# Performance work log

Hardware: AMD Instinct MI355X
Metric: run time of the kernel (lower is better)

Reference implementation:

```python
import jax, jax.numpy as jnp
import numpy as np

N = 50000
E = 800000
F_IN = 1433
H = 256
C = 7


def setup_inputs() -> dict:
    key = jax.random.key(0)
    ks = jax.random.split(key, 8)
    x = jax.random.normal(ks[0], (N, F_IN), dtype=jnp.float32)
    edge_index = jax.random.randint(ks[1], (2, E), 0, N, dtype=jnp.int32)
    # glorot init for linear weights
    def glorot(k, fan_in, fan_out):
        s = jnp.sqrt(6.0 / (fan_in + fan_out)).astype(jnp.float32)
        return jax.random.uniform(k, (fan_in, fan_out), jnp.float32, -s, s)
    W1 = glorot(ks[2], F_IN, H)
    W2 = glorot(ks[3], H, H)
    W3 = glorot(ks[4], H, C)
    b1 = jnp.zeros((H,), jnp.float32)
    b2 = jnp.zeros((H,), jnp.float32)
    b3 = jnp.zeros((C,), jnp.float32)
    return {"x": x, "edge_index": edge_index, "W1": W1, "b1": b1,
            "W2": W2, "b2": b2, "W3": W3, "b3": b3}


def _gcn_norm(edge_index, num_nodes):
    # add self-loops, edge_weight = 1, symmetric normalization
    row = jnp.concatenate([edge_index[0], jnp.arange(num_nodes, dtype=edge_index.dtype)])
    col = jnp.concatenate([edge_index[1], jnp.arange(num_nodes, dtype=edge_index.dtype)])
    w = jnp.ones(row.shape[0], dtype=jnp.float32)
    deg = jax.ops.segment_sum(w, col, num_segments=num_nodes)  # degree on target (col)
    dinv = jnp.where(deg > 0, jax.lax.rsqrt(deg), 0.0)
    norm = dinv[row] * dinv[col]  # [E+N]
    return row, col, norm


def _gcn_layer(x, W, b, row, col, norm, num_nodes):
    h = x @ W                                   # [N, F_out]
    msg = h[row] * norm[:, None]                # gather + scale, [E+N, F_out]
    out = jax.ops.segment_sum(msg, col, num_segments=num_nodes)  # scatter-add
    return out + b


def reference(x, edge_index, W1, b1, W2, b2, W3, b3):
    row, col, norm = _gcn_norm(edge_index, N)
    h = jax.nn.relu(_gcn_layer(x, W1, b1, row, col, norm, N))
    h = jax.nn.relu(_gcn_layer(h, W2, b2, row, col, norm, N))
    h = _gcn_layer(h, W3, b3, row, col, norm, N)
    return jax.nn.log_softmax(h, axis=1)
```

## Files before the change

kernel.cpp:

```cpp
#include <hip/hip_runtime.h>
#include <math.h>

#define NNODES 50000
#define NEDGES 800000
#define FIN    1433
#define KP1    1472
#define HDIM   256
#define NCLS   7
#define MPAD   50048

typedef __attribute__((ext_vector_type(8))) short short8;
typedef __attribute__((ext_vector_type(4))) float f32x4;

__device__ __forceinline__ unsigned short f2bf(float f) {
    unsigned u = __builtin_bit_cast(unsigned, f);
    u += 0x7fffu + ((u >> 16) & 1u);
    return (unsigned short)(u >> 16);
}

__device__ __forceinline__ float bf2f(unsigned short u) {
    unsigned v = ((unsigned)u) << 16;
    return __builtin_bit_cast(float, v);
}

__device__ __forceinline__ void gl2lds16(const void* g, void* l) {
    __builtin_amdgcn_global_load_lds(
        (const __attribute__((address_space(1))) unsigned int*)g,
        (__attribute__((address_space(3))) unsigned int*)l, 16, 0, 0);
}

__device__ __forceinline__ f32x4 ld4u(const float* p) {
    f32x4 v; __builtin_memcpy(&v, p, 16); return v;
}


__global__ void count_kernel(const int* __restrict__ col, int* __restrict__ cnt, int E) {
    int e = blockIdx.x * blockDim.x + threadIdx.x;
    if (e < E) atomicAdd(&cnt[col[e]], 1);
}

#define SCAN_BS 512

__global__ __launch_bounds__(SCAN_BS) void scan_part(const int* __restrict__ cnt,
                                                     int* __restrict__ bsum, int n) {
    __shared__ int red[SCAN_BS];
    int t = threadIdx.x;
    int i = blockIdx.x * SCAN_BS + t;
    red[t] = (i < n) ? cnt[i] : 0;
    __syncthreads();
    for (int off = SCAN_BS / 2; off > 0; off >>= 1) {
        if (t < off) red[t] += red[t + off];
        __syncthreads();
    }
    if (t == 0) bsum[blockIdx.x] = red[0];
}

__global__ __launch_bounds__(128) void scan_top(int* __restrict__ bsum, int nb) {
    __shared__ int s[128];
    int t = threadIdx.x;
    int v = (t < nb) ? bsum[t] : 0;
    s[t] = v;
    __syncthreads();
    for (int off = 1; off < 128; off <<= 1) {
        int u = (t >= off) ? s[t - off] : 0;
        __syncthreads();
        s[t] += u;
        __syncthreads();
    }
    if (t < nb) bsum[t] = s[t] - v;
}

__global__ __launch_bounds__(SCAN_BS) void scan_apply(const int* __restrict__ cnt,
                                                      const int* __restrict__ bsum,
                                                      int* __restrict__ rp,
                                                      float* __restrict__ dinv,
                                                      int n, int total) {
    __shared__ int s[SCAN_BS];
    int t = threadIdx.x;
    int i = blockIdx.x * SCAN_BS + t;
    int v = (i < n) ? cnt[i] : 0;
    s[t] = v;
    __syncthreads();
    for (int off = 1; off < SCAN_BS; off <<= 1) {
        int u = (t >= off) ? s[t - off] : 0;
        __syncthreads();
        s[t] += u;
        __syncthreads();
    }
    if (i < n) {
        rp[i] = bsum[blockIdx.x] + s[t] - v;
        dinv[i] = rsqrtf((float)(v + 1));
    }
    if (i == n) rp[n] = total;
}

__global__ void fill_kernel(const int* __restrict__ row, const int* __restrict__ col,
                            const int* __restrict__ rp, int* __restrict__ cur,
                            int2* __restrict__ csrw,
                            const float* __restrict__ dinv, int E) {
    int e = blockIdx.x * blockDim.x + threadIdx.x;
    if (e < E) {
        int c = col[e], r = row[e];
        int pos = rp[c] + atomicAdd(&cur[c], 1);
        csrw[pos] = make_int2(r, __float_as_int(dinv[r] * dinv[c]));
    }
}


__global__ void cast_wt2(const float* __restrict__ W1, const float* __restrict__ W2,
                         unsigned short* __restrict__ w1t, unsigned short* __restrict__ w2t) {
    int idx = blockIdx.x * blockDim.x + threadIdx.x;
    if (idx < HDIM * KP1) {
        int n = idx / KP1, k = idx % KP1;
        w1t[idx] = f2bf((k < FIN) ? W1[(size_t)k * HDIM + n] : 0.f);
    } else {
        int j = idx - HDIM * KP1;
        if (j < HDIM * HDIM) {
            int n = j / HDIM, k = j % HDIM;
            w2t[j] = f2bf(W2[(size_t)k * HDIM + n]);
        }
    }
}


__global__ __launch_bounds__(256) void gemm1_fused(const float* __restrict__ X,
                                                   const unsigned short* __restrict__ Bt,
                                                   unsigned short* __restrict__ C) {
    __shared__ __align__(16) unsigned short As[64 * 64];
    __shared__ __align__(16) unsigned short Bs[256 * 64];
    const int tid = threadIdx.x;
    const int wave = tid >> 6, lane = tid & 63;
    const int m0 = blockIdx.x * 64;
    const int wn = wave * 64;
    const int kq = lane >> 4, l16 = lane & 15;
    const int lq = lane >> 4;
    const int h  = lane & 15;

    int rowbase[4];
    #pragma unroll
    for (int i = 0; i < 4; ++i) {
        int r = m0 + wave * 16 + i * 4 + lq;
        if (r >= NNODES) r = NNODES - 1;
        rowbase[i] = r * FIN;
    }
    int aw[4];
    #pragma unroll
    for (int i = 0; i < 4; ++i) {
        int r7 = lq + 4 * (i & 1);
        aw[i] = (wave * 16 + i * 4 + lq) * 64 + (((h >> 1) ^ r7) * 8) + (h & 1) * 4;
    }

    int bo[8];
    #pragma unroll
    for (int i = 0; i < 8; ++i) {
        int c = i * 256 + tid;
        int n = c >> 3, ccg = (c & 7) ^ (n & 7);
        bo[i] = n * KP1 + ccg * 8;
    }

    int aoffb[2], boffb[2];
    #pragma unroll
    for (int ks = 0; ks < 2; ++ks) {
        int swz = ((ks * 4 + kq) ^ (l16 & 7)) * 8;
        aoffb[ks] = l16 * 64 + swz;
        boffb[ks] = (wn + l16) * 64 + swz;
    }

    f32x4 acc[4][4] = {};
    constexpr int NT = KP1 / 64;

    f32x4 fv[4];
    #pragma unroll
    for (int i = 0; i < 4; ++i) fv[i] = ld4u(&X[rowbase[i] + h * 4]);

    for (int t = 0; t < NT; ++t) {
        const int k0 = t * 64;
        #pragma unroll
        for (int i = 0; i < 8; ++i)
            gl2lds16(Bt + bo[i] + k0, &Bs[(i * 256 + tid) * 8]);
        #pragma unroll
        for (int i = 0; i < 4; ++i) {
            ushort4 pk = make_ushort4(f2bf(fv[i].x), f2bf(fv[i].y),
                                      f2bf(fv[i].z), f2bf(fv[i].w));
            *(ushort4*)&As[aw[i]] = pk;
        }
        __syncthreads();

        f32x4 nv[4];
        const bool more = (t + 1 < NT);
        if (more) {
            const int kb = k0 + 64 + h * 4;
            if (t + 2 == NT) {
                #pragma unroll
                for (int i = 0; i < 4; ++i) {
                    float a = (kb + 0 < FIN) ? X[rowbase[i] + kb + 0] : 0.f;
                    float b = (kb + 1 < FIN) ? X[rowbase[i] + kb + 1] : 0.f;
                    float c = (kb + 2 < FIN) ? X[rowbase[i] + kb + 2] : 0.f;
                    float d = (kb + 3 < FIN) ? X[rowbase[i] + kb + 3] : 0.f;
                    nv[i] = (f32x4){a, b, c, d};
                }
            } else {
                #pragma unroll
                for (int i = 0; i < 4; ++i) nv[i] = ld4u(&X[rowbase[i] + kb]);
            }
        }

        #pragma unroll
        for (int ks = 0; ks < 2; ++ks) {
            short8 af[4], bg[4];
            #pragma unroll
            for (int i = 0; i < 4; ++i) af[i] = *(const short8*)&As[i * 1024 + aoffb[ks]];
            #pragma unroll
            for (int j = 0; j < 4; ++j) bg[j] = *(const short8*)&Bs[j * 1024 + boffb[ks]];
            #pragma unroll
            for (int i = 0; i < 4; ++i)
                #pragma unroll
                for (int j = 0; j < 4; ++j)
                    acc[i][j] = __builtin_amdgcn_mfma_f32_16x16x32_bf16(af[i], bg[j], acc[i][j], 0, 0, 0);
        }
        __syncthreads();
        if (more) {
            #pragma unroll
            for (int i = 0; i < 4; ++i) fv[i] = nv[i];
        }
    }

    #pragma unroll
    for (int i = 0; i < 4; ++i) {
        int gm_base = m0 + i * 16 + (lane >> 4) * 4;
        #pragma unroll
        for (int r = 0; r < 4; ++r) {
            int gm = gm_base + r;
            if (gm < NNODES) {
                #pragma unroll
                for (int j = 0; j < 4; ++j) {
                    int gn = wn + j * 16 + l16;
                    C[(size_t)gm * HDIM + gn] = f2bf(acc[i][j][r]);
                }
            }
        }
    }
}


__global__ __launch_bounds__(256) void gemm2_lds(const unsigned short* __restrict__ A,
                                                 const unsigned short* __restrict__ Bt,
                                                 unsigned short* __restrict__ C) {
    __shared__ __align__(16) unsigned short As[64 * 64];
    __shared__ __align__(16) unsigned short Bs[256 * 64];
    const int tid = threadIdx.x;
    const int wave = tid >> 6, lane = tid & 63;
    const int m0 = blockIdx.x * 64;
    const int wn = wave * 64;
    const int kq = lane >> 4, l16 = lane & 15;

    int ao[2];
    #pragma unroll
    for (int i = 0; i < 2; ++i) {
        int c = i * 256 + tid;
        int m = c >> 3, ccg = (c & 7) ^ (m & 7);
        ao[i] = (m0 + m) * HDIM + ccg * 8;
    }
    int bo[8];
    #pragma unroll
    for (int i = 0; i < 8; ++i) {
        int c = i * 256 + tid;
        int n = c >> 3, ccg = (c & 7) ^ (n & 7);
        bo[i] = n * HDIM + ccg * 8;
    }
    int aoffb[2], boffb[2];
    #pragma unroll
    for (int ks = 0; ks < 2; ++ks) {
        int swz = ((ks * 4 + kq) ^ (l16 & 7)) * 8;
        aoffb[ks] = l16 * 64 + swz;
        boffb[ks] = (wn + l16) * 64 + swz;
    }

    f32x4 acc[4][4] = {};
    #pragma unroll
    for (int k0 = 0; k0 < HDIM; k0 += 64) {
        #pragma unroll
        for (int i = 0; i < 2; ++i) gl2lds16(A + ao[i] + k0, &As[(i * 256 + tid) * 8]);
        #pragma unroll
        for (int i = 0; i < 8; ++i) gl2lds16(Bt + bo[i] + k0, &Bs[(i * 256 + tid) * 8]);
        __syncthreads();
        #pragma unroll
        for (int ks = 0; ks < 2; ++ks) {
            short8 af[4], bg[4];
            #pragma unroll
            for (int i = 0; i < 4; ++i) af[i] = *(const short8*)&As[i * 1024 + aoffb[ks]];
            #pragma unroll
            for (int j = 0; j < 4; ++j) bg[j] = *(const short8*)&Bs[j * 1024 + boffb[ks]];
            #pragma unroll
            for (int i = 0; i < 4; ++i)
                #pragma unroll
                for (int j = 0; j < 4; ++j)
                    acc[i][j] = __builtin_amdgcn_mfma_f32_16x16x32_bf16(af[i], bg[j], acc[i][j], 0, 0, 0);
        }
        __syncthreads();
    }

    #pragma unroll
    for (int i = 0; i < 4; ++i) {
        int gm_base = m0 + i * 16 + (lane >> 4) * 4;
        #pragma unroll
        for (int r = 0; r < 4; ++r) {
            int gm = gm_base + r;
            if (gm < NNODES) {
                #pragma unroll
                for (int j = 0; j < 4; ++j) {
                    int gn = wn + j * 16 + l16;
                    C[(size_t)gm * HDIM + gn] = f2bf(acc[i][j][r]);
                }
            }
        }
    }
}


__device__ __forceinline__ void aggregate_row(const ushort4* __restrict__ h, int lane,
                                              int p, int p1,
                                              const int2* __restrict__ csrw,
                                              float& ax, float& ay, float& az, float& aw) {
    for (; p + 8 <= p1; p += 8) {
        int2 e[8];
        #pragma unroll
        for (int j = 0; j < 8; ++j) e[j] = csrw[p + j];
        ushort4 t[8];
        #pragma unroll
        for (int j = 0; j < 8; ++j) t[j] = h[e[j].x * 64 + lane];
        #pragma unroll
        for (int j = 0; j < 8; ++j) {
            float w = __int_as_float(e[j].y);
            ax += w * bf2f(t[j].x); ay += w * bf2f(t[j].y);
            az += w * bf2f(t[j].z); aw += w * bf2f(t[j].w);
        }
    }
    if (p + 4 <= p1) {
        int2 e[4];
        #pragma unroll
        for (int j = 0; j < 4; ++j) e[j] = csrw[p + j];
        ushort4 t[4];
        #pragma unroll
        for (int j = 0; j < 4; ++j) t[j] = h[e[j].x * 64 + lane];
        #pragma unroll
        for (int j = 0; j < 4; ++j) {
            float w = __int_as_float(e[j].y);
            ax += w * bf2f(t[j].x); ay += w * bf2f(t[j].y);
            az += w * bf2f(t[j].z); aw += w * bf2f(t[j].w);
        }
        p += 4;
    }
    for (; p < p1; ++p) {
        int2 e = csrw[p];
        float w = __int_as_float(e.y);
        ushort4 t = h[e.x * 64 + lane];
        ax += w * bf2f(t.x); ay += w * bf2f(t.y); az += w * bf2f(t.z); aw += w * bf2f(t.w);
    }
}


__global__ __launch_bounds__(256) void agg_kernel(const ushort4* __restrict__ h,
                                                  ushort4* __restrict__ out,
                                                  const float* __restrict__ dinv,
                                                  const int* __restrict__ rp,
                                                  const int2* __restrict__ csrw,
                                                  const float* __restrict__ bias,
                                                  int n) {
    int node = blockIdx.x * 4 + (threadIdx.x >> 6);
    int lane = threadIdx.x & 63;
    if (node >= n) return;
    float di = dinv[node];
    float sw = di * di;
    ushort4 hv = h[node * 64 + lane];
    float ax = sw * bf2f(hv.x), ay = sw * bf2f(hv.y);
    float az = sw * bf2f(hv.z), aw = sw * bf2f(hv.w);
    aggregate_row(h, lane, rp[node], rp[node + 1], csrw, ax, ay, az, aw);
    float4 b = ((const float4*)bias)[lane];
    ax = fmaxf(ax + b.x, 0.f); ay = fmaxf(ay + b.y, 0.f);
    az = fmaxf(az + b.z, 0.f); aw = fmaxf(aw + b.w, 0.f);
    out[node * 64 + lane] = make_ushort4(f2bf(ax), f2bf(ay), f2bf(az), f2bf(aw));
}


__global__ __launch_bounds__(256) void agg2_mm3_kernel(const ushort4* __restrict__ h,
                                                       float* __restrict__ h3,
                                                       const float* __restrict__ dinv,
                                                       const int* __restrict__ rp,
                                                       const int2* __restrict__ csrw,
                                                       const float* __restrict__ bias,
                                                       const float* __restrict__ W3,
                                                       int n) {
    __shared__ __align__(16) float Ws[NCLS * HDIM];
    int tid = threadIdx.x;
    for (int i = tid; i < NCLS * HDIM; i += 256)
        Ws[i] = W3[(i & 255) * NCLS + (i >> 8)];
    __syncthreads();

    int node = blockIdx.x * 4 + (tid >> 6);
    int lane = tid & 63;
    if (node >= n) return;
    float di = dinv[node];
    float sw = di * di;
    ushort4 hv = h[node * 64 + lane];
    float ax = sw * bf2f(hv.x), ay = sw * bf2f(hv.y);
    float az = sw * bf2f(hv.z), aw = sw * bf2f(hv.w);
    aggregate_row(h, lane, rp[node], rp[node + 1], csrw, ax, ay, az, aw);
    float4 b = ((const float4*)bias)[lane];
    ax = fmaxf(ax + b.x, 0.f); ay = fmaxf(ay + b.y, 0.f);
    az = fmaxf(az + b.z, 0.f); aw = fmaxf(aw + b.w, 0.f);

    float p7[NCLS];
    #pragma unroll
    for (int c = 0; c < NCLS; ++c) {
        float4 w4 = *(const float4*)&Ws[c * HDIM + 4 * lane];
        p7[c] = ax * w4.x + ay * w4.y + az * w4.z + aw * w4.w;
    }
    #pragma unroll
    for (int c = 0; c < NCLS; ++c)
        for (int off = 32; off > 0; off >>= 1) p7[c] += __shfl_down(p7[c], off);
    if (lane == 0) {
        #pragma unroll
        for (int c = 0; c < NCLS; ++c) h3[node * NCLS + c] = p7[c];
    }
}


__global__ void final_kernel(const float* __restrict__ h3, const float* __restrict__ dinv,
                             const int* __restrict__ rp, const int2* __restrict__ csrw,
                             const float* __restrict__ b3, float* __restrict__ out, int n) {
    int i = blockIdx.x * blockDim.x + threadIdx.x;
    if (i >= n) return;
    float di = dinv[i];
    float sw = di * di;
    float acc[NCLS];
    #pragma unroll
    for (int c = 0; c < NCLS; ++c) acc[c] = sw * h3[i * NCLS + c];
    int p = rp[i], p1 = rp[i + 1];
    for (; p + 4 <= p1; p += 4) {
        int2 e0 = csrw[p], e1 = csrw[p + 1], e2 = csrw[p + 2], e3 = csrw[p + 3];
        float w0 = __int_as_float(e0.y), w1 = __int_as_float(e1.y);
        float w2 = __int_as_float(e2.y), w3 = __int_as_float(e3.y);
        #pragma unroll
        for (int c = 0; c < NCLS; ++c)
            acc[c] += w0 * h3[e0.x * NCLS + c] + w1 * h3[e1.x * NCLS + c]
                    + w2 * h3[e2.x * NCLS + c] + w3 * h3[e3.x * NCLS + c];
    }
    for (; p < p1; ++p) {
        int2 e = csrw[p];
        float wg = __int_as_float(e.y);
        #pragma unroll
        for (int c = 0; c < NCLS; ++c) acc[c] += wg * h3[e.x * NCLS + c];
    }
    float mx = -1e30f;
    #pragma unroll
    for (int c = 0; c < NCLS; ++c) { acc[c] += b3[c]; mx = fmaxf(mx, acc[c]); }
    float sum = 0.f;
    #pragma unroll
    for (int c = 0; c < NCLS; ++c) sum += expf(acc[c] - mx);
    float lse = mx + logf(sum);
    #pragma unroll
    for (int c = 0; c < NCLS; ++c) out[i * NCLS + c] = acc[c] - lse;
}


extern "C" void kernel_launch(void* const* d_in, const int* in_sizes, int n_in,
                              void* d_out, int out_size, void* d_ws, size_t ws_size,
                              hipStream_t stream) {
    const float* x  = (const float*)d_in[0];
    const int*   ei = (const int*)d_in[1];
    const float* W1 = (const float*)d_in[2];
    const float* b1 = (const float*)d_in[3];
    const float* W2 = (const float*)d_in[4];
    const float* b2 = (const float*)d_in[5];
    const float* W3 = (const float*)d_in[6];
    const float* b3 = (const float*)d_in[7];
    float* out = (float*)d_out;
    const int* row = ei;
    const int* col = ei + NEDGES;

    char* w = (char*)d_ws;
    auto alloc = [&](size_t b) { void* p = (void*)w; w += (b + 255) & ~(size_t)255; return p; };
    int*   cnt  = (int*)alloc(NNODES * 4);
    int*   cur  = (int*)alloc(NNODES * 4);
    int*   rp   = (int*)alloc((NNODES + 1) * 4);
    float* dinv = (float*)alloc(NNODES * 4);
    int*   bsum = (int*)alloc(128 * 4);
    int2*  csrw = (int2*)alloc((size_t)NEDGES * 8);
    unsigned short* w1t  = (unsigned short*)alloc((size_t)HDIM * KP1 * 2);
    unsigned short* w2t  = (unsigned short*)alloc((size_t)HDIM * HDIM * 2);
    unsigned short* h_bf = (unsigned short*)alloc((size_t)MPAD * HDIM * 2);
    unsigned short* a_bf = (unsigned short*)alloc((size_t)MPAD * HDIM * 2);
    float* h3 = (float*)alloc((size_t)NNODES * NCLS * 4);

    const size_t cpad = ((size_t)NNODES * 4 + 255) & ~(size_t)255;
    hipMemsetAsync(cnt, 0, cpad + (size_t)NNODES * 4, stream);

    count_kernel<<<(NEDGES + 255) / 256, 256, 0, stream>>>(col, cnt, NEDGES);
    const int nsb = (NNODES + SCAN_BS - 1) / SCAN_BS;
    scan_part <<<nsb, SCAN_BS, 0, stream>>>(cnt, bsum, NNODES);
    scan_top  <<<1, 128, 0, stream>>>(bsum, nsb);
    scan_apply<<<nsb, SCAN_BS, 0, stream>>>(cnt, bsum, rp, dinv, NNODES, NEDGES);
    fill_kernel<<<(NEDGES + 255) / 256, 256, 0, stream>>>(row, col, rp, cur, csrw, dinv, NEDGES);

    cast_wt2<<<(HDIM * KP1 + HDIM * HDIM + 255) / 256, 256, 0, stream>>>(W1, W2, w1t, w2t);

    gemm1_fused<<<MPAD / 64, 256, 0, stream>>>(x, w1t, h_bf);
    agg_kernel<<<(NNODES + 3) / 4, 256, 0, stream>>>((const ushort4*)h_bf, (ushort4*)a_bf,
                                                     dinv, rp, csrw, b1, NNODES);
    gemm2_lds<<<MPAD / 64, 256, 0, stream>>>(a_bf, w2t, h_bf);
    agg2_mm3_kernel<<<(NNODES + 3) / 4, 256, 0, stream>>>((const ushort4*)h_bf, h3,
                                                          dinv, rp, csrw, b2, W3, NNODES);
    final_kernel<<<(NNODES + 255) / 256, 256, 0, stream>>>(h3, dinv, rp, csrw, b3, out, NNODES);
}
```

Baseline: 676.8 us.

## Split aggregation wave into half-waves with 16-byte gathers; pad h3 to 8 floats

The aggregation kernels now split each 64-lane wave into two halves. Each half processes alternate edges and gathers 16-byte bf16 vectors, and the halves are combined with a cross-half shuffle. This halves the number of gather instructions per edge row and doubles the edges in flight per wave. The layer-3 output is stored padded to 8 floats, so the final kernel can use float4 gathers. The 0.5 scale in the padded store compensates for the duplicated reduction across both halves. The edge count and weight-cast kernels are merged into one launch, which removes one launch. The cost is more complex tail handling, with zero-weight dummy loads for odd edge counts.

```diff
diff --git a/kernel.cpp b/kernel.cpp
--- a/kernel.cpp
+++ b/kernel.cpp
@@ -34,9 +34,29 @@
 }
 
 
-__global__ void count_kernel(const int* __restrict__ col, int* __restrict__ cnt, int E) {
-    int e = blockIdx.x * blockDim.x + threadIdx.x;
-    if (e < E) atomicAdd(&cnt[col[e]], 1);
+#define NB_COUNT 3125
+#define NB_CAST  1728
+
+__global__ void count_cast(const int* __restrict__ col, int* __restrict__ cnt,
+                           const float* __restrict__ W1, const float* __restrict__ W2,
+                           unsigned short* __restrict__ w1t, unsigned short* __restrict__ w2t) {
+    int b = blockIdx.x;
+    if (b < NB_COUNT) {
+        int e = b * 256 + threadIdx.x;
+        if (e < NEDGES) atomicAdd(&cnt[col[e]], 1);
+    } else {
+        int idx = (b - NB_COUNT) * 256 + threadIdx.x;
+        if (idx < HDIM * KP1) {
+            int n = idx / KP1, k = idx % KP1;
+            w1t[idx] = f2bf((k < FIN) ? W1[(size_t)k * HDIM + n] : 0.f);
+        } else {
+            int j = idx - HDIM * KP1;
+            if (j < HDIM * HDIM) {
+                int n = j / HDIM, k = j % HDIM;
+                w2t[j] = f2bf(W2[(size_t)k * HDIM + n]);
+            }
+        }
+    }
 }
 
 #define SCAN_BS 512
@@ -103,22 +123,6 @@
         int c = col[e], r = row[e];
         int pos = rp[c] + atomicAdd(&cur[c], 1);
         csrw[pos] = make_int2(r, __float_as_int(dinv[r] * dinv[c]));
-    }
-}
-
-
-__global__ void cast_wt2(const float* __restrict__ W1, const float* __restrict__ W2,
-                         unsigned short* __restrict__ w1t, unsigned short* __restrict__ w2t) {
-    int idx = blockIdx.x * blockDim.x + threadIdx.x;
-    if (idx < HDIM * KP1) {
-        int n = idx / KP1, k = idx % KP1;
-        w1t[idx] = f2bf((k < FIN) ? W1[(size_t)k * HDIM + n] : 0.f);
-    } else {
-        int j = idx - HDIM * KP1;
-        if (j < HDIM * HDIM) {
-            int n = j / HDIM, k = j % HDIM;
-            w2t[j] = f2bf(W2[(size_t)k * HDIM + n]);
-        }
     }
 }
 
@@ -318,50 +322,66 @@
 }
 
 
-__device__ __forceinline__ void aggregate_row(const ushort4* __restrict__ h, int lane,
-                                              int p, int p1,
-                                              const int2* __restrict__ csrw,
-                                              float& ax, float& ay, float& az, float& aw) {
-    for (; p + 8 <= p1; p += 8) {
+__device__ __forceinline__ void agg_pair(const short8* __restrict__ hh, int node,
+                                         int hl, int q, float sw,
+                                         int p, int p1,
+                                         const int2* __restrict__ csrw,
+                                         float acc[8]) {
+    int idx; float w;
+    if (q == 0) { idx = node; w = sw; }
+    else if (p < p1) { int2 e = csrw[p]; idx = e.x; w = __int_as_float(e.y); }
+    else { idx = node; w = 0.f; }
+    {
+        short8 t = hh[idx * 32 + hl];
+        #pragma unroll
+        for (int d = 0; d < 8; ++d) acc[d] = w * bf2f((unsigned short)t[d]);
+    }
+    p += 1;
+    for (; p + 16 <= p1; p += 16) {
         int2 e[8];
         #pragma unroll
-        for (int j = 0; j < 8; ++j) e[j] = csrw[p + j];
-        ushort4 t[8];
-        #pragma unroll
-        for (int j = 0; j < 8; ++j) t[j] = h[e[j].x * 64 + lane];
+        for (int j = 0; j < 8; ++j) e[j] = csrw[p + 2 * j + q];
+        short8 t[8];
+        #pragma unroll
+        for (int j = 0; j < 8; ++j) t[j] = hh[e[j].x * 32 + hl];
         #pragma unroll
         for (int j = 0; j < 8; ++j) {
-            float w = __int_as_float(e[j].y);
-            ax += w * bf2f(t[j].x); ay += w * bf2f(t[j].y);
-            az += w * bf2f(t[j].z); aw += w * bf2f(t[j].w);
-        }
-    }
-    if (p + 4 <= p1) {
+            float wj = __int_as_float(e[j].y);
+            #pragma unroll
+            for (int d = 0; d < 8; ++d) acc[d] += wj * bf2f((unsigned short)t[j][d]);
+        }
+    }
+    if (p + 8 <= p1) {
         int2 e[4];
         #pragma unroll
-        for (int j = 0; j < 4; ++j) e[j] = csrw[p + j];
-        ushort4 t[4];
-        #pragma unroll
-        for (int j = 0; j < 4; ++j) t[j] = h[e[j].x * 64 + lane];
+        for (int j = 0; j < 4; ++j) e[j] = csrw[p + 2 * j + q];
+        short8 t[4];
+        #pragma unroll
+        for (int j = 0; j < 4; ++j) t[j] = hh[e[j].x * 32 + hl];
         #pragma unroll
         for (int j = 0; j < 4; ++j) {
-            float w = __int_as_float(e[j].y);
-            ax += w * bf2f(t[j].x); ay += w * bf2f(t[j].y);
-            az += w * bf2f(t[j].z); aw += w * bf2f(t[j].w);
-        }
-        p += 4;
-    }
-    for (; p < p1; ++p) {
-        int2 e = csrw[p];
-        float w = __int_as_float(e.y);
-        ushort4 t = h[e.x * 64 + lane];
-        ax += w * bf2f(t.x); ay += w * bf2f(t.y); az += w * bf2f(t.z); aw += w * bf2f(t.w);
-    }
-}
-
-
-__global__ __launch_bounds__(256) void agg_kernel(const ushort4* __restrict__ h,
-                                                  ushort4* __restrict__ out,
+            float wj = __int_as_float(e[j].y);
+            #pragma unroll
+            for (int d = 0; d < 8; ++d) acc[d] += wj * bf2f((unsigned short)t[j][d]);
+        }
+        p += 8;
+    }
+    for (; p < p1; p += 2) {
+        int pe = p + q;
+        int ix; float wj;
+        if (pe < p1) { int2 e = csrw[pe]; ix = e.x; wj = __int_as_float(e.y); }
+        else { ix = node; wj = 0.f; }
+        short8 t = hh[ix * 32 + hl];
+        #pragma unroll
+        for (int d = 0; d < 8; ++d) acc[d] += wj * bf2f((unsigned short)t[d]);
+    }
+    #pragma unroll
+    for (int d = 0; d < 8; ++d) acc[d] += __shfl_xor(acc[d], 32);
+}
+
+
+__global__ __launch_bounds__(256) void agg_kernel(const short8* __restrict__ hh,
+                                                  short8* __restrict__ out,
                                                   const float* __restrict__ dinv,
                                                   const int* __restrict__ rp,
                                                   const int2* __restrict__ csrw,
@@ -370,21 +390,29 @@
     int node = blockIdx.x * 4 + (threadIdx.x >> 6);
     int lane = threadIdx.x & 63;
     if (node >= n) return;
+    int hl = lane & 31, q = lane >> 5;
     float di = dinv[node];
-    float sw = di * di;
-    ushort4 hv = h[node * 64 + lane];
-    float ax = sw * bf2f(hv.x), ay = sw * bf2f(hv.y);
-    float az = sw * bf2f(hv.z), aw = sw * bf2f(hv.w);
-    aggregate_row(h, lane, rp[node], rp[node + 1], csrw, ax, ay, az, aw);
-    float4 b = ((const float4*)bias)[lane];
-    ax = fmaxf(ax + b.x, 0.f); ay = fmaxf(ay + b.y, 0.f);
-    az = fmaxf(az + b.z, 0.f); aw = fmaxf(aw + b.w, 0.f);
-    out[node * 64 + lane] = make_ushort4(f2bf(ax), f2bf(ay), f2bf(az), f2bf(aw));
-}
-
-
-__global__ __launch_bounds__(256) void agg2_mm3_kernel(const ushort4* __restrict__ h,
-                                                       float* __restrict__ h3,
+    float acc[8];
+    agg_pair(hh, node, hl, q, di * di, rp[node], rp[node + 1], csrw, acc);
+    if (q == 0) {
+        const float4* b4 = (const float4*)bias;
+        float4 ba = b4[hl * 2], bb = b4[hl * 2 + 1];
+        short8 pk;
+        pk[0] = (short)f2bf(fmaxf(acc[0] + ba.x, 0.f));
+        pk[1] = (short)f2bf(fmaxf(acc[1] + ba.y, 0.f));
+        pk[2] = (short)f2bf(fmaxf(acc[2] + ba.z, 0.f));
+        pk[3] = (short)f2bf(fmaxf(acc[3] + ba.w, 0.f));
+        pk[4] = (short)f2bf(fmaxf(acc[4] + bb.x, 0.f));
+        pk[5] = (short)f2bf(fmaxf(acc[5] + bb.y, 0.f));
+        pk[6] = (short)f2bf(fmaxf(acc[6] + bb.z, 0.f));
+        pk[7] = (short)f2bf(fmaxf(acc[7] + bb.w, 0.f));
+        out[node * 32 + hl] = pk;
+    }
+}
+
+
+__global__ __launch_bounds__(256) void agg2_mm3_kernel(const short8* __restrict__ hh,
+                                                       float* __restrict__ h3p,
                                                        const float* __restrict__ dinv,
                                                        const int* __restrict__ rp,
                                                        const int2* __restrict__ csrw,
@@ -400,58 +428,74 @@
     int node = blockIdx.x * 4 + (tid >> 6);
     int lane = tid & 63;
     if (node >= n) return;
+    int hl = lane & 31, q = lane >> 5;
     float di = dinv[node];
-    float sw = di * di;
-    ushort4 hv = h[node * 64 + lane];
-    float ax = sw * bf2f(hv.x), ay = sw * bf2f(hv.y);
-    float az = sw * bf2f(hv.z), aw = sw * bf2f(hv.w);
-    aggregate_row(h, lane, rp[node], rp[node + 1], csrw, ax, ay, az, aw);
-    float4 b = ((const float4*)bias)[lane];
-    ax = fmaxf(ax + b.x, 0.f); ay = fmaxf(ay + b.y, 0.f);
-    az = fmaxf(az + b.z, 0.f); aw = fmaxf(aw + b.w, 0.f);
+    float acc[8];
+    agg_pair(hh, node, hl, q, di * di, rp[node], rp[node + 1], csrw, acc);
+    const float4* b4 = (const float4*)bias;
+    float4 ba = b4[hl * 2], bb = b4[hl * 2 + 1];
+    float a[8];
+    a[0] = fmaxf(acc[0] + ba.x, 0.f); a[1] = fmaxf(acc[1] + ba.y, 0.f);
+    a[2] = fmaxf(acc[2] + ba.z, 0.f); a[3] = fmaxf(acc[3] + ba.w, 0.f);
+    a[4] = fmaxf(acc[4] + bb.x, 0.f); a[5] = fmaxf(acc[5] + bb.y, 0.f);
+    a[6] = fmaxf(acc[6] + bb.z, 0.f); a[7] = fmaxf(acc[7] + bb.w, 0.f);
 
     float p7[NCLS];
     #pragma unroll
     for (int c = 0; c < NCLS; ++c) {
-        float4 w4 = *(const float4*)&Ws[c * HDIM + 4 * lane];
-        p7[c] = ax * w4.x + ay * w4.y + az * w4.z + aw * w4.w;
+        const float4* w4 = (const float4*)&Ws[c * HDIM + hl * 8];
+        float4 wa = w4[0], wb = w4[1];
+        p7[c] = a[0] * wa.x + a[1] * wa.y + a[2] * wa.z + a[3] * wa.w
+              + a[4] * wb.x + a[5] * wb.y + a[6] * wb.z + a[7] * wb.w;
     }
     #pragma unroll
     for (int c = 0; c < NCLS; ++c)
         for (int off = 32; off > 0; off >>= 1) p7[c] += __shfl_down(p7[c], off);
     if (lane == 0) {
-        #pragma unroll
-        for (int c = 0; c < NCLS; ++c) h3[node * NCLS + c] = p7[c];
-    }
-}
-
-
-__global__ void final_kernel(const float* __restrict__ h3, const float* __restrict__ dinv,
+        float4 lo = make_float4(0.5f * p7[0], 0.5f * p7[1], 0.5f * p7[2], 0.5f * p7[3]);
+        float4 hi = make_float4(0.5f * p7[4], 0.5f * p7[5], 0.5f * p7[6], 0.f);
+        *(float4*)&h3p[node * 8]     = lo;
+        *(float4*)&h3p[node * 8 + 4] = hi;
+    }
+}
+
+
+__global__ void final_kernel(const float* __restrict__ h3p, const float* __restrict__ dinv,
                              const int* __restrict__ rp, const int2* __restrict__ csrw,
                              const float* __restrict__ b3, float* __restrict__ out, int n) {
     int i = blockIdx.x * blockDim.x + threadIdx.x;
     if (i >= n) return;
+    const float4* H = (const float4*)h3p;
     float di = dinv[i];
     float sw = di * di;
-    float acc[NCLS];
-    #pragma unroll
-    for (int c = 0; c < NCLS; ++c) acc[c] = sw * h3[i * NCLS + c];
+    float4 su = H[i * 2], sv = H[i * 2 + 1];
+    float a0 = sw * su.x, a1 = sw * su.y, a2 = sw * su.z, a3 = sw * su.w;
+    float a4 = sw * sv.x, a5 = sw * sv.y, a6 = sw * sv.z;
     int p = rp[i], p1 = rp[i + 1];
     for (; p + 4 <= p1; p += 4) {
         int2 e0 = csrw[p], e1 = csrw[p + 1], e2 = csrw[p + 2], e3 = csrw[p + 3];
         float w0 = __int_as_float(e0.y), w1 = __int_as_float(e1.y);
         float w2 = __int_as_float(e2.y), w3 = __int_as_float(e3.y);
-        #pragma unroll
-        for (int c = 0; c < NCLS; ++c)
-            acc[c] += w0 * h3[e0.x * NCLS + c] + w1 * h3[e1.x * NCLS + c]
-                    + w2 * h3[e2.x * NCLS + c] + w3 * h3[e3.x * NCLS + c];
+        float4 u0 = H[e0.x * 2], v0 = H[e0.x * 2 + 1];
+        float4 u1 = H[e1.x * 2], v1 = H[e1.x * 2 + 1];
+        float4 u2 = H[e2.x * 2], v2 = H[e2.x * 2 + 1];
+        float4 u3 = H[e3.x * 2], v3 = H[e3.x * 2 + 1];
+        a0 += w0 * u0.x + w1 * u1.x + w2 * u2.x + w3 * u3.x;
+        a1 += w0 * u0.y + w1 * u1.y + w2 * u2.y + w3 * u3.y;
+        a2 += w0 * u0.z + w1 * u1.z + w2 * u2.z + w3 * u3.z;
+        a3 += w0 * u0.w + w1 * u1.w + w2 * u2.w + w3 * u3.w;
+        a4 += w0 * v0.x + w1 * v1.x + w2 * v2.x + w3 * v3.x;
+        a5 += w0 * v0.y + w1 * v1.y + w2 * v2.y + w3 * v3.y;
+        a6 += w0 * v0.z + w1 * v1.z + w2 * v2.z + w3 * v3.z;
     }
     for (; p < p1; ++p) {
         int2 e = csrw[p];
         float wg = __int_as_float(e.y);
-        #pragma unroll
-        for (int c = 0; c < NCLS; ++c) acc[c] += wg * h3[e.x * NCLS + c];
-    }
+        float4 u = H[e.x * 2], v = H[e.x * 2 + 1];
+        a0 += wg * u.x; a1 += wg * u.y; a2 += wg * u.z; a3 += wg * u.w;
+        a4 += wg * v.x; a5 += wg * v.y; a6 += wg * v.z;
+    }
+    float acc[NCLS] = {a0, a1, a2, a3, a4, a5, a6};
     float mx = -1e30f;
     #pragma unroll
     for (int c = 0; c < NCLS; ++c) { acc[c] += b3[c]; mx = fmaxf(mx, acc[c]); }
@@ -491,25 +535,23 @@
     unsigned short* w2t  = (unsigned short*)alloc((size_t)HDIM * HDIM * 2);
     unsigned short* h_bf = (unsigned short*)alloc((size_t)MPAD * HDIM * 2);
     unsigned short* a_bf = (unsigned short*)alloc((size_t)MPAD * HDIM * 2);
-    float* h3 = (float*)alloc((size_t)NNODES * NCLS * 4);
+    float* h3p = (float*)alloc((size_t)NNODES * 8 * 4);
 
     const size_t cpad = ((size_t)NNODES * 4 + 255) & ~(size_t)255;
     hipMemsetAsync(cnt, 0, cpad + (size_t)NNODES * 4, stream);
 
-    count_kernel<<<(NEDGES + 255) / 256, 256, 0, stream>>>(col, cnt, NEDGES);
+    count_cast<<<NB_COUNT + NB_CAST, 256, 0, stream>>>(col, cnt, W1, W2, w1t, w2t);
     const int nsb = (NNODES + SCAN_BS - 1) / SCAN_BS;
     scan_part <<<nsb, SCAN_BS, 0, stream>>>(cnt, bsum, NNODES);
     scan_top  <<<1, 128, 0, stream>>>(bsum, nsb);
     scan_apply<<<nsb, SCAN_BS, 0, stream>>>(cnt, bsum, rp, dinv, NNODES, NEDGES);
     fill_kernel<<<(NEDGES + 255) / 256, 256, 0, stream>>>(row, col, rp, cur, csrw, dinv, NEDGES);
 
-    cast_wt2<<<(HDIM * KP1 + HDIM * HDIM + 255) / 256, 256, 0, stream>>>(W1, W2, w1t, w2t);
-
     gemm1_fused<<<MPAD / 64, 256, 0, stream>>>(x, w1t, h_bf);
-    agg_kernel<<<(NNODES + 3) / 4, 256, 0, stream>>>((const ushort4*)h_bf, (ushort4*)a_bf,
+    agg_kernel<<<(NNODES + 3) / 4, 256, 0, stream>>>((const short8*)h_bf, (short8*)a_bf,
                                                      dinv, rp, csrw, b1, NNODES);
     gemm2_lds<<<MPAD / 64, 256, 0, stream>>>(a_bf, w2t, h_bf);
-    agg2_mm3_kernel<<<(NNODES + 3) / 4, 256, 0, stream>>>((const ushort4*)h_bf, h3,
+    agg2_mm3_kernel<<<(NNODES + 3) / 4, 256, 0, stream>>>((const short8*)h_bf, h3p,
                                                           dinv, rp, csrw, b2, W3, NNODES);
-    final_kernel<<<(NNODES + 255) / 256, 256, 0, stream>>>(h3, dinv, rp, csrw, b3, out, NNODES);
-}
+    final_kernel<<<(NNODES + 255) / 256, 256, 0, stream>>>(h3p, dinv, rp, csrw, b3, out, NNODES);
+}
```

After: 721.1 us. 1.07x slower.

## Merge preprocessing kernels into GEMM1 and pad class logits to float4

Applied to the files above, without the earlier changes.

Packs edge counting and the weight cast into one launch, and folds the scan_top step into scan_apply: each block sums the preceding block totals itself. The CSR fill now runs as extra blocks inside the first GEMM launch, so fill and GEMM1 can overlap. The 7-class intermediate is padded to 8 floats so the final aggregation reads it with aligned float4 loads. This cuts launch count and serialization, at the cost of a heavier fused kernel, whose shared-memory footprint is also reserved by the fill blocks, and a serial prefix loop per scan block.

```diff
diff --git a/kernel.cpp b/kernel.cpp
--- a/kernel.cpp
+++ b/kernel.cpp
@@ -8,6 +8,7 @@
 #define HDIM   256
 #define NCLS   7
 #define MPAD   50048
+#define G1B    782
 
 typedef __attribute__((ext_vector_type(8))) short short8;
 typedef __attribute__((ext_vector_type(4))) float f32x4;
@@ -34,12 +35,33 @@
 }
 
 
-__global__ void count_kernel(const int* __restrict__ col, int* __restrict__ cnt, int E) {
-    int e = blockIdx.x * blockDim.x + threadIdx.x;
-    if (e < E) atomicAdd(&cnt[col[e]], 1);
+#define NB_COUNT 3125
+#define NB_CAST  1728
+
+__global__ void count_cast(const int* __restrict__ col, int* __restrict__ cnt,
+                           const float* __restrict__ W1, const float* __restrict__ W2,
+                           unsigned short* __restrict__ w1t, unsigned short* __restrict__ w2t) {
+    int b = blockIdx.x;
+    if (b < NB_COUNT) {
+        int e = b * 256 + threadIdx.x;
+        if (e < NEDGES) atomicAdd(&cnt[col[e]], 1);
+    } else {
+        int idx = (b - NB_COUNT) * 256 + threadIdx.x;
+        if (idx < HDIM * KP1) {
+            int n = idx / KP1, k = idx % KP1;
+            w1t[idx] = f2bf((k < FIN) ? W1[(size_t)k * HDIM + n] : 0.f);
+        } else {
+            int j = idx - HDIM * KP1;
+            if (j < HDIM * HDIM) {
+                int n = j / HDIM, k = j % HDIM;
+                w2t[j] = f2bf(W2[(size_t)k * HDIM + n]);
+            }
+        }
+    }
 }
 
 #define SCAN_BS 512
+#define NSB     98
 
 __global__ __launch_bounds__(SCAN_BS) void scan_part(const int* __restrict__ cnt,
                                                      int* __restrict__ bsum, int n) {
@@ -55,32 +77,25 @@
     if (t == 0) bsum[blockIdx.x] = red[0];
 }
 
-__global__ __launch_bounds__(128) void scan_top(int* __restrict__ bsum, int nb) {
-    __shared__ int s[128];
-    int t = threadIdx.x;
-    int v = (t < nb) ? bsum[t] : 0;
-    s[t] = v;
-    __syncthreads();
-    for (int off = 1; off < 128; off <<= 1) {
-        int u = (t >= off) ? s[t - off] : 0;
-        __syncthreads();
-        s[t] += u;
-        __syncthreads();
-    }
-    if (t < nb) bsum[t] = s[t] - v;
-}
-
 __global__ __launch_bounds__(SCAN_BS) void scan_apply(const int* __restrict__ cnt,
                                                       const int* __restrict__ bsum,
                                                       int* __restrict__ rp,
                                                       float* __restrict__ dinv,
                                                       int n, int total) {
     __shared__ int s[SCAN_BS];
+    __shared__ int bs[128];
+    __shared__ int base;
     int t = threadIdx.x;
+    if (t < 128) bs[t] = (t < NSB) ? bsum[t] : 0;
     int i = blockIdx.x * SCAN_BS + t;
     int v = (i < n) ? cnt[i] : 0;
     s[t] = v;
     __syncthreads();
+    if (t == 0) {
+        int acc = 0;
+        for (int j = 0; j < blockIdx.x; ++j) acc += bs[j];
+        base = acc;
+    }
     for (int off = 1; off < SCAN_BS; off <<= 1) {
         int u = (t >= off) ? s[t - off] : 0;
         __syncthreads();
@@ -88,46 +103,35 @@
         __syncthreads();
     }
     if (i < n) {
-        rp[i] = bsum[blockIdx.x] + s[t] - v;
+        rp[i] = base + s[t] - v;
         dinv[i] = rsqrtf((float)(v + 1));
     }
     if (i == n) rp[n] = total;
 }
 
-__global__ void fill_kernel(const int* __restrict__ row, const int* __restrict__ col,
-                            const int* __restrict__ rp, int* __restrict__ cur,
-                            int2* __restrict__ csrw,
-                            const float* __restrict__ dinv, int E) {
-    int e = blockIdx.x * blockDim.x + threadIdx.x;
-    if (e < E) {
-        int c = col[e], r = row[e];
-        int pos = rp[c] + atomicAdd(&cur[c], 1);
-        csrw[pos] = make_int2(r, __float_as_int(dinv[r] * dinv[c]));
-    }
-}
-
-
-__global__ void cast_wt2(const float* __restrict__ W1, const float* __restrict__ W2,
-                         unsigned short* __restrict__ w1t, unsigned short* __restrict__ w2t) {
-    int idx = blockIdx.x * blockDim.x + threadIdx.x;
-    if (idx < HDIM * KP1) {
-        int n = idx / KP1, k = idx % KP1;
-        w1t[idx] = f2bf((k < FIN) ? W1[(size_t)k * HDIM + n] : 0.f);
-    } else {
-        int j = idx - HDIM * KP1;
-        if (j < HDIM * HDIM) {
-            int n = j / HDIM, k = j % HDIM;
-            w2t[j] = f2bf(W2[(size_t)k * HDIM + n]);
-        }
-    }
-}
-
-
-__global__ __launch_bounds__(256) void gemm1_fused(const float* __restrict__ X,
-                                                   const unsigned short* __restrict__ Bt,
-                                                   unsigned short* __restrict__ C) {
+
+__global__ __launch_bounds__(256) void fill_gemm1(const float* __restrict__ X,
+                                                  const unsigned short* __restrict__ Bt,
+                                                  unsigned short* __restrict__ C,
+                                                  const int* __restrict__ row,
+                                                  const int* __restrict__ col,
+                                                  const int* __restrict__ rp,
+                                                  int* __restrict__ cur,
+                                                  int2* __restrict__ csrw,
+                                                  const float* __restrict__ dinv) {
     __shared__ __align__(16) unsigned short As[64 * 64];
     __shared__ __align__(16) unsigned short Bs[256 * 64];
+
+    if (blockIdx.x >= G1B) {
+        int e = (blockIdx.x - G1B) * 256 + threadIdx.x;
+        if (e < NEDGES) {
+            int c = col[e], r = row[e];
+            int pos = rp[c] + atomicAdd(&cur[c], 1);
+            csrw[pos] = make_int2(r, __float_as_int(dinv[r] * dinv[c]));
+        }
+        return;
+    }
+
     const int tid = threadIdx.x;
     const int wave = tid >> 6, lane = tid & 63;
     const int m0 = blockIdx.x * 64;
@@ -384,7 +388,7 @@
 
 
 __global__ __launch_bounds__(256) void agg2_mm3_kernel(const ushort4* __restrict__ h,
-                                                       float* __restrict__ h3,
+                                                       float* __restrict__ h3p,
                                                        const float* __restrict__ dinv,
                                                        const int* __restrict__ rp,
                                                        const int2* __restrict__ csrw,
@@ -420,38 +424,48 @@
     for (int c = 0; c < NCLS; ++c)
         for (int off = 32; off > 0; off >>= 1) p7[c] += __shfl_down(p7[c], off);
     if (lane == 0) {
-        #pragma unroll
-        for (int c = 0; c < NCLS; ++c) h3[node * NCLS + c] = p7[c];
-    }
-}
-
-
-__global__ void final_kernel(const float* __restrict__ h3, const float* __restrict__ dinv,
+        *(float4*)&h3p[node * 8]     = make_float4(p7[0], p7[1], p7[2], p7[3]);
+        *(float4*)&h3p[node * 8 + 4] = make_float4(p7[4], p7[5], p7[6], 0.f);
+    }
+}
+
+
+__global__ void final_kernel(const float* __restrict__ h3p, const float* __restrict__ dinv,
                              const int* __restrict__ rp, const int2* __restrict__ csrw,
                              const float* __restrict__ b3, float* __restrict__ out, int n) {
     int i = blockIdx.x * blockDim.x + threadIdx.x;
     if (i >= n) return;
+    const float4* H = (const float4*)h3p;
     float di = dinv[i];
     float sw = di * di;
-    float acc[NCLS];
-    #pragma unroll
-    for (int c = 0; c < NCLS; ++c) acc[c] = sw * h3[i * NCLS + c];
+    float4 su = H[i * 2], sv = H[i * 2 + 1];
+    float a0 = sw * su.x, a1 = sw * su.y, a2 = sw * su.z, a3 = sw * su.w;
+    float a4 = sw * sv.x, a5 = sw * sv.y, a6 = sw * sv.z;
     int p = rp[i], p1 = rp[i + 1];
     for (; p + 4 <= p1; p += 4) {
         int2 e0 = csrw[p], e1 = csrw[p + 1], e2 = csrw[p + 2], e3 = csrw[p + 3];
         float w0 = __int_as_float(e0.y), w1 = __int_as_float(e1.y);
         float w2 = __int_as_float(e2.y), w3 = __int_as_float(e3.y);
-        #pragma unroll
-        for (int c = 0; c < NCLS; ++c)
-            acc[c] += w0 * h3[e0.x * NCLS + c] + w1 * h3[e1.x * NCLS + c]
-                    + w2 * h3[e2.x * NCLS + c] + w3 * h3[e3.x * NCLS + c];
+        float4 u0 = H[e0.x * 2], v0 = H[e0.x * 2 + 1];
+        float4 u1 = H[e1.x * 2], v1 = H[e1.x * 2 + 1];
+        float4 u2 = H[e2.x * 2], v2 = H[e2.x * 2 + 1];
+        float4 u3 = H[e3.x * 2], v3 = H[e3.x * 2 + 1];
+        a0 += w0 * u0.x + w1 * u1.x + w2 * u2.x + w3 * u3.x;
+        a1 += w0 * u0.y + w1 * u1.y + w2 * u2.y + w3 * u3.y;
+        a2 += w0 * u0.z + w1 * u1.z + w2 * u2.z + w3 * u3.z;
+        a3 += w0 * u0.w + w1 * u1.w + w2 * u2.w + w3 * u3.w;
+        a4 += w0 * v0.x + w1 * v1.x + w2 * v2.x + w3 * v3.x;
+        a5 += w0 * v0.y + w1 * v1.y + w2 * v2.y + w3 * v3.y;
+        a6 += w0 * v0.z + w1 * v1.z + w2 * v2.z + w3 * v3.z;
     }
     for (; p < p1; ++p) {
         int2 e = csrw[p];
         float wg = __int_as_float(e.y);
-        #pragma unroll
-        for (int c = 0; c < NCLS; ++c) acc[c] += wg * h3[e.x * NCLS + c];
-    }
+        float4 u = H[e.x * 2], v = H[e.x * 2 + 1];
+        a0 += wg * u.x; a1 += wg * u.y; a2 += wg * u.z; a3 += wg * u.w;
+        a4 += wg * v.x; a5 += wg * v.y; a6 += wg * v.z;
+    }
+    float acc[NCLS] = {a0, a1, a2, a3, a4, a5, a6};
     float mx = -1e30f;
     #pragma unroll
     for (int c = 0; c < NCLS; ++c) { acc[c] += b3[c]; mx = fmaxf(mx, acc[c]); }
@@ -491,25 +505,21 @@
     unsigned short* w2t  = (unsigned short*)alloc((size_t)HDIM * HDIM * 2);
     unsigned short* h_bf = (unsigned short*)alloc((size_t)MPAD * HDIM * 2);
     unsigned short* a_bf = (unsigned short*)alloc((size_t)MPAD * HDIM * 2);
-    float* h3 = (float*)alloc((size_t)NNODES * NCLS * 4);
+    float* h3p = (float*)alloc((size_t)NNODES * 8 * 4);
 
     const size_t cpad = ((size_t)NNODES * 4 + 255) & ~(size_t)255;
     hipMemsetAsync(cnt, 0, cpad + (size_t)NNODES * 4, stream);
 
-    count_kernel<<<(NEDGES + 255) / 256, 256, 0, stream>>>(col, cnt, NEDGES);
-    const int nsb = (NNODES + SCAN_BS - 1) / SCAN_BS;
-    scan_part <<<nsb, SCAN_BS, 0, stream>>>(cnt, bsum, NNODES);
-    scan_top  <<<1, 128, 0, stream>>>(bsum, nsb);
-    scan_apply<<<nsb, SCAN_BS, 0, stream>>>(cnt, bsum, rp, dinv, NNODES, NEDGES);
-    fill_kernel<<<(NEDGES + 255) / 256, 256, 0, stream>>>(row, col, rp, cur, csrw, dinv, NEDGES);
-
-    cast_wt2<<<(HDIM * KP1 + HDIM * HDIM + 255) / 256, 256, 0, stream>>>(W1, W2, w1t, w2t);
-
-    gemm1_fused<<<MPAD / 64, 256, 0, stream>>>(x, w1t, h_bf);
+    count_cast<<<NB_COUNT + NB_CAST, 256, 0, stream>>>(col, cnt, W1, W2, w1t, w2t);
+    scan_part <<<NSB, SCAN_BS, 0, stream>>>(cnt, bsum, NNODES);
+    scan_apply<<<NSB, SCAN_BS, 0, stream>>>(cnt, bsum, rp, dinv, NNODES, NEDGES);
+
+    fill_gemm1<<<G1B + NB_COUNT, 256, 0, stream>>>(x, w1t, h_bf, row, col, rp, cur, csrw, dinv);
+
     agg_kernel<<<(NNODES + 3) / 4, 256, 0, stream>>>((const ushort4*)h_bf, (ushort4*)a_bf,
                                                      dinv, rp, csrw, b1, NNODES);
     gemm2_lds<<<MPAD / 64, 256, 0, stream>>>(a_bf, w2t, h_bf);
-    agg2_mm3_kernel<<<(NNODES + 3) / 4, 256, 0, stream>>>((const ushort4*)h_bf, h3,
+    agg2_mm3_kernel<<<(NNODES + 3) / 4, 256, 0, stream>>>((const ushort4*)h_bf, h3p,
                                                           dinv, rp, csrw, b2, W3, NNODES);
-    final_kernel<<<(NNODES + 255) / 256, 256, 0, stream>>>(h3, dinv, rp, csrw, b3, out, NNODES);
-}
+    final_kernel<<<(NNODES + 255) / 256, 256, 0, stream>>>(h3p, dinv, rp, csrw, b3, out, NNODES);
+}
```

Result: faster. 643.2 us (-5.0%).
